# Performance work log

Hardware: AMD Instinct MI355X
Metric: run time of the kernel (lower is better)

The kernel has to match this reference:

```python
import jax, jax.numpy as jnp
import numpy as np

N, K, D = 16384, 2048, 512

def setup_inputs() -> dict:
    key = jax.random.key(0)
    kx, kmu, kstd = jax.random.split(key, 3)
    x = jax.random.normal(kx, (N, D), dtype=jnp.float32)
    mu = jax.random.normal(kmu, (K, D), dtype=jnp.float32)
    std = jax.random.uniform(kstd, (K, D), dtype=jnp.float32)  # positive so log(sum(std)) is defined
    return {"x": x, "mu": mu, "std": std}

def reference(x, mu, std):
    x_sq = jnp.sum(x * x, axis=1)                      # [N]
    mu_sq = jnp.sum(mu * mu, axis=1)                   # [K]
    sqdist = x_sq[:, None] - 2.0 * (x @ mu.T) + mu_sq[None, :]  # [N, K]
    denom = 2.0 * jnp.sum(std * std, axis=1) + 1e-8    # [K]
    log_std_sum = jnp.log(jnp.sum(std, axis=1))        # [K]
    half_log_2pi = 0.5 * jnp.log(jnp.asarray(2.0 * np.pi, dtype=x.dtype))
    return -sqdist / denom[None, :] - log_std_sum[None, :] - half_log_2pi
```

## Files before the change

kernel.cpp:

```cpp
#include <hip/hip_runtime.h>
#include <hip/hip_bf16.h>
#include <stdint.h>

#define NN 16384
#define KK 2048
#define DD 512

typedef __bf16 bf16x8 __attribute__((ext_vector_type(8)));
typedef float f32x4 __attribute__((ext_vector_type(4)));
typedef unsigned short ushort_t;
typedef ushort_t us8 __attribute__((ext_vector_type(8)));

#define AS1(p) ((const __attribute__((address_space(1))) void*)(p))
#define AS3(p) ((__attribute__((address_space(3))) void*)(p))

#define FENCE() asm volatile("" ::: "memory")
#define SBAR()  do { FENCE(); __builtin_amdgcn_s_barrier(); FENCE(); } while (0)
#define WAITVM0() asm volatile("s_waitcnt vmcnt(0)" ::: "memory")

__device__ inline ushort_t f2bf(float f) {
  uint32_t u = __float_as_uint(f);
  u += 0x7fffu + ((u >> 16) & 1u);
  return (ushort_t)(u >> 16);
}


__global__ __launch_bounds__(256) void prep_x(const float* __restrict__ x,
                                              ushort_t* __restrict__ xb,
                                              float* __restrict__ x_sq) {
  const int wave = threadIdx.x >> 6;
  const int lane = threadIdx.x & 63;
  const int row = blockIdx.x * 4 + wave;
  const float* xr = x + (size_t)row * DD + lane * 8;
  float4 v0 = *reinterpret_cast<const float4*>(xr);
  float4 v1 = *reinterpret_cast<const float4*>(xr + 4);
  float s = v0.x*v0.x + v0.y*v0.y + v0.z*v0.z + v0.w*v0.w
          + v1.x*v1.x + v1.y*v1.y + v1.z*v1.z + v1.w*v1.w;
  us8 o;
  o[0]=f2bf(v0.x); o[1]=f2bf(v0.y); o[2]=f2bf(v0.z); o[3]=f2bf(v0.w);
  o[4]=f2bf(v1.x); o[5]=f2bf(v1.y); o[6]=f2bf(v1.z); o[7]=f2bf(v1.w);

  const int br = row >> 8, m = (row >> 4) & 15, r = row & 15;
  const int kt = lane >> 3, cc2 = lane & 7, ks = cc2 >> 2, slot = cc2 & 3;
  size_t off = (size_t)(br * 8 + kt) * 16384 + (m * 2 + ks) * 512 + slot * 128 + r * 8;
  *reinterpret_cast<us8*>(xb + off) = o;

  #pragma unroll
  for (int offs = 32; offs; offs >>= 1) s += __shfl_xor(s, offs, 64);
  if (lane == 0) x_sq[row] = s;
}

__global__ __launch_bounds__(256) void prep_mu(const float* __restrict__ mu,
                                               const float* __restrict__ sd,
                                               ushort_t* __restrict__ mub,
                                               float* __restrict__ inv_denom,
                                               float* __restrict__ beta) {
  const int wave = threadIdx.x >> 6;
  const int lane = threadIdx.x & 63;
  const int row = blockIdx.x * 4 + wave;
  const float* mr = mu + (size_t)row * DD + lane * 8;
  float4 v0 = *reinterpret_cast<const float4*>(mr);
  float4 v1 = *reinterpret_cast<const float4*>(mr + 4);
  float musq = v0.x*v0.x + v0.y*v0.y + v0.z*v0.z + v0.w*v0.w
             + v1.x*v1.x + v1.y*v1.y + v1.z*v1.z + v1.w*v1.w;
  us8 o;
  o[0]=f2bf(v0.x); o[1]=f2bf(v0.y); o[2]=f2bf(v0.z); o[3]=f2bf(v0.w);
  o[4]=f2bf(v1.x); o[5]=f2bf(v1.y); o[6]=f2bf(v1.z); o[7]=f2bf(v1.w);

  const int bc = row >> 8, cB = (row >> 4) & 15, r = row & 15;
  const int kt = lane >> 3, cc2 = lane & 7, ks = cc2 >> 2, slot = cc2 & 3;
  size_t off = (size_t)(bc * 8 + kt) * 16384 + (cB * 2 + ks) * 512 + slot * 128 + r * 8;
  *reinterpret_cast<us8*>(mub + off) = o;

  const float* sr = sd + (size_t)row * DD + lane * 8;
  float4 s0 = *reinterpret_cast<const float4*>(sr);
  float4 s1 = *reinterpret_cast<const float4*>(sr + 4);
  float ssum = s0.x + s0.y + s0.z + s0.w + s1.x + s1.y + s1.z + s1.w;
  float ssq  = s0.x*s0.x + s0.y*s0.y + s0.z*s0.z + s0.w*s0.w
             + s1.x*s1.x + s1.y*s1.y + s1.z*s1.z + s1.w*s1.w;
  #pragma unroll
  for (int offs = 32; offs; offs >>= 1) {
    musq += __shfl_xor(musq, offs, 64);
    ssum += __shfl_xor(ssum, offs, 64);
    ssq  += __shfl_xor(ssq,  offs, 64);
  }
  if (lane == 0) {
    float idn = 1.0f / (2.0f * ssq + 1e-8f);
    inv_denom[row] = idn;
    beta[row] = musq * idn + logf(ssum) + 0.91893853320467274f;
  }
}

__global__ __launch_bounds__(512, 2) void gemm_eval(const ushort_t* __restrict__ xb,
                                                    const ushort_t* __restrict__ mub,
                                                    const float* __restrict__ x_sq,
                                                    const float* __restrict__ inv_denom,
                                                    const float* __restrict__ beta,
                                                    float* __restrict__ out) {
  __shared__ __align__(16) ushort_t As[2][16384];
  __shared__ __align__(16) ushort_t Bs[2][16384];

  const int t0 = threadIdx.x;
  const int lane = t0 & 63;
  const int w = t0 >> 6;
  const int wrow = w >> 2;
  const int wcol = w & 3;

  const int bid = blockIdx.x;
  const int swz = (bid & 7) * 64 + (bid >> 3);
  const int bm = swz >> 3, bn = swz & 7;

  const ushort_t* Ag = xb  + (size_t)bm * (8 * 16384);
  const ushort_t* Bg = mub + (size_t)bn * (8 * 16384);

  f32x4 acc[8][4];
  #pragma unroll
  for (int mmi = 0; mmi < 8; ++mmi)
    #pragma unroll
    for (int cc = 0; cc < 4; ++cc)
      acc[mmi][cc] = (f32x4){0.f, 0.f, 0.f, 0.f};

#define STAGE(kt, dbuf) do {                                                        \
    const ushort_t* as_ = Ag + (size_t)(kt) * 16384;                                \
    const ushort_t* bs_ = Bg + (size_t)(kt) * 16384;                                \
    ushort_t* ad_ = &As[dbuf][0];                                                   \
    ushort_t* bd_ = &Bs[dbuf][0];                                                   \
    __builtin_amdgcn_global_load_lds(AS1(as_ + t0*8),        AS3(ad_ + t0*8),        16, 0, 0); \
    __builtin_amdgcn_global_load_lds(AS1(as_ + (t0+512)*8),  AS3(ad_ + (t0+512)*8),  16, 0, 0); \
    __builtin_amdgcn_global_load_lds(AS1(as_ + (t0+1024)*8), AS3(ad_ + (t0+1024)*8), 16, 0, 0); \
    __builtin_amdgcn_global_load_lds(AS1(as_ + (t0+1536)*8), AS3(ad_ + (t0+1536)*8), 16, 0, 0); \
    __builtin_amdgcn_global_load_lds(AS1(bs_ + t0*8),        AS3(bd_ + t0*8),        16, 0, 0); \
    __builtin_amdgcn_global_load_lds(AS1(bs_ + (t0+512)*8),  AS3(bd_ + (t0+512)*8),  16, 0, 0); \
    __builtin_amdgcn_global_load_lds(AS1(bs_ + (t0+1024)*8), AS3(bd_ + (t0+1024)*8), 16, 0, 0); \
    __builtin_amdgcn_global_load_lds(AS1(bs_ + (t0+1536)*8), AS3(bd_ + (t0+1536)*8), 16, 0, 0); \
  } while (0)

  STAGE(0, 0);
  WAITVM0();
  SBAR();

  for (int t = 0; t < 8; ++t) {
    const ushort_t* Acur = &As[t & 1][0];
    const ushort_t* Bcur = &Bs[t & 1][0];
    bf16x8 bfrag[4][2];
    #pragma unroll
    for (int q = 0; q < 4; ++q) {
      bf16x8 af[2][2];
      #pragma unroll
      for (int i = 0; i < 2; ++i)
        #pragma unroll
        for (int ks = 0; ks < 2; ++ks)
          af[i][ks] = *reinterpret_cast<const bf16x8*>(
              Acur + ((wrow * 8 + q * 2 + i) * 2 + ks) * 512 + lane * 8);
      if (q == 0) {
        #pragma unroll
        for (int cc = 0; cc < 4; ++cc)
          #pragma unroll
          for (int ks = 0; ks < 2; ++ks)
            bfrag[cc][ks] = *reinterpret_cast<const bf16x8*>(
                Bcur + ((wcol * 4 + cc) * 2 + ks) * 512 + lane * 8);
        if (t < 7) STAGE(t + 1, (t + 1) & 1);
      }
      SBAR();
      __builtin_amdgcn_s_setprio(1);
      #pragma unroll
      for (int i = 0; i < 2; ++i)
        #pragma unroll
        for (int cc = 0; cc < 4; ++cc)
          #pragma unroll
          for (int ks = 0; ks < 2; ++ks)
            acc[q * 2 + i][cc] = __builtin_amdgcn_mfma_f32_16x16x32_bf16(
                af[i][ks], bfrag[cc][ks], acc[q * 2 + i][cc], 0, 0, 0);
      __builtin_amdgcn_s_setprio(0);
      if (q == 3) WAITVM0();
      SBAR();
    }
  }

  const int rl = lane & 15, rh = lane >> 4;
  const int colbase = bn * 256 + wcol * 64;
  float inv[4], bet[4];
  #pragma unroll
  for (int cc = 0; cc < 4; ++cc) {
    inv[cc] = inv_denom[colbase + cc * 16 + rl];
    bet[cc] = beta[colbase + cc * 16 + rl];
  }
  #pragma unroll
  for (int mmi = 0; mmi < 8; ++mmi) {
    const int nb = bm * 256 + wrow * 128 + mmi * 16 + rh * 4;
    #pragma unroll
    for (int reg = 0; reg < 4; ++reg) {
      const int n = nb + reg;
      const float xs = x_sq[n];
      float* op = out + (size_t)n * KK + colbase;
      #pragma unroll
      for (int cc = 0; cc < 4; ++cc)
        op[cc * 16 + rl] = (2.0f * acc[mmi][cc][reg] - xs) * inv[cc] - bet[cc];
    }
  }
#undef STAGE
}

extern "C" void kernel_launch(void* const* d_in, const int* in_sizes, int n_in,
                              void* d_out, int out_size, void* d_ws, size_t ws_size,
                              hipStream_t stream) {
  const float* x   = (const float*)d_in[0];
  const float* mu  = (const float*)d_in[1];
  const float* sd  = (const float*)d_in[2];
  float* out = (float*)d_out;

  char* ws = (char*)d_ws;
  ushort_t* xb        = (ushort_t*)(ws);
  ushort_t* mub       = (ushort_t*)(ws + 16777216);
  float*    x_sq      = (float*)(ws + 18874368);
  float*    inv_denom = (float*)(ws + 18939904);
  float*    beta      = (float*)(ws + 18948096);

  prep_x<<<NN / 4, 256, 0, stream>>>(x, xb, x_sq);
  prep_mu<<<KK / 4, 256, 0, stream>>>(mu, sd, mub, inv_denom, beta);
  gemm_eval<<<(NN / 256) * (KK / 256), 512, 0, stream>>>(xb, mub, x_sq, inv_denom, beta, out);
}
```

Measured before the change: 202.2 us.

## Switch GEMM to 4-stage K pipeline with smaller K tiles

Reorganizes the bf16 packed layout of x and mu into 32-wide K slices of 128-row images, and rewrites the GEMM main loop into a 4-buffer ring that keeps three K tiles in flight. A and B loads for the next-next tile are issued in separate halves of each step, with partial vmcnt waits instead of full drains. The aim is to hide global-to-LDS latency better than the old double buffer with its full wait each tile. In exchange it adds more barriers per unit of MFMA work (16 steps with 3 barriers each) and more complex vmcnt accounting.

```diff
diff --git a/kernel.cpp b/kernel.cpp
--- a/kernel.cpp
+++ b/kernel.cpp
@@ -13,10 +13,8 @@
 
 #define AS1(p) ((const __attribute__((address_space(1))) void*)(p))
 #define AS3(p) ((__attribute__((address_space(3))) void*)(p))
-
 #define FENCE() asm volatile("" ::: "memory")
 #define SBAR()  do { FENCE(); __builtin_amdgcn_s_barrier(); FENCE(); } while (0)
-#define WAITVM0() asm volatile("s_waitcnt vmcnt(0)" ::: "memory")
 
 __device__ inline ushort_t f2bf(float f) {
   uint32_t u = __float_as_uint(f);
@@ -40,9 +38,9 @@
   o[0]=f2bf(v0.x); o[1]=f2bf(v0.y); o[2]=f2bf(v0.z); o[3]=f2bf(v0.w);
   o[4]=f2bf(v1.x); o[5]=f2bf(v1.y); o[6]=f2bf(v1.z); o[7]=f2bf(v1.w);
 
-  const int br = row >> 8, m = (row >> 4) & 15, r = row & 15;
-  const int kt = lane >> 3, cc2 = lane & 7, ks = cc2 >> 2, slot = cc2 & 3;
-  size_t off = (size_t)(br * 8 + kt) * 16384 + (m * 2 + ks) * 512 + slot * 128 + r * 8;
+  const int br = row >> 7, m = (row >> 4) & 7, r = row & 15;
+  const int kt = lane >> 2, slot = lane & 3;
+  size_t off = ((size_t)(br * 16 + kt)) * 4096 + m * 512 + slot * 128 + r * 8;
   *reinterpret_cast<us8*>(xb + off) = o;
 
   #pragma unroll
@@ -67,9 +65,9 @@
   o[0]=f2bf(v0.x); o[1]=f2bf(v0.y); o[2]=f2bf(v0.z); o[3]=f2bf(v0.w);
   o[4]=f2bf(v1.x); o[5]=f2bf(v1.y); o[6]=f2bf(v1.z); o[7]=f2bf(v1.w);
 
-  const int bc = row >> 8, cB = (row >> 4) & 15, r = row & 15;
-  const int kt = lane >> 3, cc2 = lane & 7, ks = cc2 >> 2, slot = cc2 & 3;
-  size_t off = (size_t)(bc * 8 + kt) * 16384 + (cB * 2 + ks) * 512 + slot * 128 + r * 8;
+  const int bc = row >> 7, m = (row >> 4) & 7, r = row & 15;
+  const int kt = lane >> 2, slot = lane & 3;
+  size_t off = ((size_t)(bc * 16 + kt)) * 4096 + m * 512 + slot * 128 + r * 8;
   *reinterpret_cast<us8*>(mub + off) = o;
 
   const float* sr = sd + (size_t)row * DD + lane * 8;
@@ -97,8 +95,7 @@
                                                     const float* __restrict__ inv_denom,
                                                     const float* __restrict__ beta,
                                                     float* __restrict__ out) {
-  __shared__ __align__(16) ushort_t As[2][16384];
-  __shared__ __align__(16) ushort_t Bs[2][16384];
+  __shared__ __align__(16) ushort_t lds[4][16384];
 
   const int t0 = threadIdx.x;
   const int lane = t0 & 63;
@@ -110,72 +107,76 @@
   const int swz = (bid & 7) * 64 + (bid >> 3);
   const int bm = swz >> 3, bn = swz & 7;
 
-  const ushort_t* Ag = xb  + (size_t)bm * (8 * 16384);
-  const ushort_t* Bg = mub + (size_t)bn * (8 * 16384);
+  const ushort_t* Aimg0 = xb  + ((size_t)(bm * 2 + 0) * 16) * 4096;
+  const ushort_t* Aimg1 = xb  + ((size_t)(bm * 2 + 1) * 16) * 4096;
+  const ushort_t* Bimg0 = mub + ((size_t)(bn * 2 + 0) * 16) * 4096;
+  const ushort_t* Bimg1 = mub + ((size_t)(bn * 2 + 1) * 16) * 4096;
 
   f32x4 acc[8][4];
   #pragma unroll
-  for (int mmi = 0; mmi < 8; ++mmi)
+  for (int mm = 0; mm < 8; ++mm)
     #pragma unroll
     for (int cc = 0; cc < 4; ++cc)
-      acc[mmi][cc] = (f32x4){0.f, 0.f, 0.f, 0.f};
-
-#define STAGE(kt, dbuf) do {                                                        \
-    const ushort_t* as_ = Ag + (size_t)(kt) * 16384;                                \
-    const ushort_t* bs_ = Bg + (size_t)(kt) * 16384;                                \
-    ushort_t* ad_ = &As[dbuf][0];                                                   \
-    ushort_t* bd_ = &Bs[dbuf][0];                                                   \
-    __builtin_amdgcn_global_load_lds(AS1(as_ + t0*8),        AS3(ad_ + t0*8),        16, 0, 0); \
-    __builtin_amdgcn_global_load_lds(AS1(as_ + (t0+512)*8),  AS3(ad_ + (t0+512)*8),  16, 0, 0); \
-    __builtin_amdgcn_global_load_lds(AS1(as_ + (t0+1024)*8), AS3(ad_ + (t0+1024)*8), 16, 0, 0); \
-    __builtin_amdgcn_global_load_lds(AS1(as_ + (t0+1536)*8), AS3(ad_ + (t0+1536)*8), 16, 0, 0); \
-    __builtin_amdgcn_global_load_lds(AS1(bs_ + t0*8),        AS3(bd_ + t0*8),        16, 0, 0); \
-    __builtin_amdgcn_global_load_lds(AS1(bs_ + (t0+512)*8),  AS3(bd_ + (t0+512)*8),  16, 0, 0); \
-    __builtin_amdgcn_global_load_lds(AS1(bs_ + (t0+1024)*8), AS3(bd_ + (t0+1024)*8), 16, 0, 0); \
-    __builtin_amdgcn_global_load_lds(AS1(bs_ + (t0+1536)*8), AS3(bd_ + (t0+1536)*8), 16, 0, 0); \
+      acc[mm][cc] = (f32x4){0.f, 0.f, 0.f, 0.f};
+
+#define ISSUE_A(kt_, buf_) do {                                                                   \
+    __builtin_amdgcn_global_load_lds(AS1(Aimg0 + (size_t)(kt_) * 4096 + t0 * 8),                  \
+                                     AS3(&lds[buf_][0] + t0 * 8), 16, 0, 0);                      \
+    __builtin_amdgcn_global_load_lds(AS1(Aimg1 + (size_t)(kt_) * 4096 + t0 * 8),                  \
+                                     AS3(&lds[buf_][4096] + t0 * 8), 16, 0, 0);                   \
   } while (0)
-
-  STAGE(0, 0);
-  WAITVM0();
+#define ISSUE_B(kt_, buf_) do {                                                                   \
+    __builtin_amdgcn_global_load_lds(AS1(Bimg0 + (size_t)(kt_) * 4096 + t0 * 8),                  \
+                                     AS3(&lds[buf_][8192] + t0 * 8), 16, 0, 0);                   \
+    __builtin_amdgcn_global_load_lds(AS1(Bimg1 + (size_t)(kt_) * 4096 + t0 * 8),                  \
+                                     AS3(&lds[buf_][12288] + t0 * 8), 16, 0, 0);                  \
+  } while (0)
+
+#define TILE_BODY(t_, doIssue_, WAITASM) do {                                                     \
+    const int buf_ = (t_) & 3;                                                                    \
+    const ushort_t* Ab_ = &lds[buf_][wrow * 4096];                                                \
+    const ushort_t* Bb_ = &lds[buf_][8192 + (wcol >> 1) * 4096 + (wcol & 1) * 2048];              \
+    bf16x8 af_[4], bf_[4];                                                                        \
+    _Pragma("unroll") for (int i = 0; i < 4; ++i)                                                 \
+      af_[i] = *reinterpret_cast<const bf16x8*>(Ab_ + i * 512 + lane * 8);                        \
+    _Pragma("unroll") for (int c = 0; c < 4; ++c)                                                 \
+      bf_[c] = *reinterpret_cast<const bf16x8*>(Bb_ + c * 512 + lane * 8);                        \
+    if (doIssue_) ISSUE_A((t_) + 3, ((t_) + 3) & 3);                                              \
+    SBAR();                                                                                       \
+    __builtin_amdgcn_s_setprio(1);                                                                \
+    _Pragma("unroll") for (int i = 0; i < 4; ++i)                                                 \
+      _Pragma("unroll") for (int c = 0; c < 4; ++c)                                               \
+        acc[i][c] = __builtin_amdgcn_mfma_f32_16x16x32_bf16(af_[i], bf_[c], acc[i][c], 0, 0, 0);  \
+    __builtin_amdgcn_s_setprio(0);                                                                \
+    SBAR();                                                                                       \
+    _Pragma("unroll") for (int i = 0; i < 4; ++i)                                                 \
+      af_[i] = *reinterpret_cast<const bf16x8*>(Ab_ + (4 + i) * 512 + lane * 8);                  \
+    if (doIssue_) ISSUE_B((t_) + 3, ((t_) + 3) & 3);                                              \
+    SBAR();                                                                                       \
+    __builtin_amdgcn_s_setprio(1);                                                                \
+    _Pragma("unroll") for (int i = 0; i < 4; ++i)                                                 \
+      _Pragma("unroll") for (int c = 0; c < 4; ++c)                                               \
+        acc[4 + i][c] = __builtin_amdgcn_mfma_f32_16x16x32_bf16(af_[i], bf_[c], acc[4 + i][c], 0, 0, 0); \
+    __builtin_amdgcn_s_setprio(0);                                                                \
+    WAITASM;                                                                                      \
+    SBAR();                                                                                       \
+  } while (0)
+
+  ISSUE_A(0, 0); ISSUE_B(0, 0);
+  ISSUE_A(1, 1); ISSUE_B(1, 1);
+  ISSUE_A(2, 2); ISSUE_B(2, 2);
+  asm volatile("s_waitcnt vmcnt(8)" ::: "memory");
   SBAR();
 
-  for (int t = 0; t < 8; ++t) {
-    const ushort_t* Acur = &As[t & 1][0];
-    const ushort_t* Bcur = &Bs[t & 1][0];
-    bf16x8 bfrag[4][2];
-    #pragma unroll
-    for (int q = 0; q < 4; ++q) {
-      bf16x8 af[2][2];
-      #pragma unroll
-      for (int i = 0; i < 2; ++i)
-        #pragma unroll
-        for (int ks = 0; ks < 2; ++ks)
-          af[i][ks] = *reinterpret_cast<const bf16x8*>(
-              Acur + ((wrow * 8 + q * 2 + i) * 2 + ks) * 512 + lane * 8);
-      if (q == 0) {
-        #pragma unroll
-        for (int cc = 0; cc < 4; ++cc)
-          #pragma unroll
-          for (int ks = 0; ks < 2; ++ks)
-            bfrag[cc][ks] = *reinterpret_cast<const bf16x8*>(
-                Bcur + ((wcol * 4 + cc) * 2 + ks) * 512 + lane * 8);
-        if (t < 7) STAGE(t + 1, (t + 1) & 1);
-      }
-      SBAR();
-      __builtin_amdgcn_s_setprio(1);
-      #pragma unroll
-      for (int i = 0; i < 2; ++i)
-        #pragma unroll
-        for (int cc = 0; cc < 4; ++cc)
-          #pragma unroll
-          for (int ks = 0; ks < 2; ++ks)
-            acc[q * 2 + i][cc] = __builtin_amdgcn_mfma_f32_16x16x32_bf16(
-                af[i][ks], bfrag[cc][ks], acc[q * 2 + i][cc], 0, 0, 0);
-      __builtin_amdgcn_s_setprio(0);
-      if (q == 3) WAITVM0();
-      SBAR();
-    }
-  }
+  for (int t = 0; t < 13; ++t)
+    TILE_BODY(t, 1, asm volatile("s_waitcnt vmcnt(8)" ::: "memory"));
+  TILE_BODY(13, 0, asm volatile("s_waitcnt vmcnt(4)" ::: "memory"));
+  TILE_BODY(14, 0, asm volatile("s_waitcnt vmcnt(0)" ::: "memory"));
+  TILE_BODY(15, 0, (void)0);
+
+#undef TILE_BODY
+#undef ISSUE_A
+#undef ISSUE_B
 
   const int rl = lane & 15, rh = lane >> 4;
   const int colbase = bn * 256 + wcol * 64;
@@ -186,8 +187,8 @@
     bet[cc] = beta[colbase + cc * 16 + rl];
   }
   #pragma unroll
-  for (int mmi = 0; mmi < 8; ++mmi) {
-    const int nb = bm * 256 + wrow * 128 + mmi * 16 + rh * 4;
+  for (int mm = 0; mm < 8; ++mm) {
+    const int nb = bm * 256 + wrow * 128 + mm * 16 + rh * 4;
     #pragma unroll
     for (int reg = 0; reg < 4; ++reg) {
       const int n = nb + reg;
@@ -195,10 +196,9 @@
       float* op = out + (size_t)n * KK + colbase;
       #pragma unroll
       for (int cc = 0; cc < 4; ++cc)
-        op[cc * 16 + rl] = (2.0f * acc[mmi][cc][reg] - xs) * inv[cc] - bet[cc];
+        op[cc * 16 + rl] = (2.0f * acc[mm][cc][reg] - xs) * inv[cc] - bet[cc];
     }
   }
-#undef STAGE
 }
 
 extern "C" void kernel_launch(void* const* d_in, const int* in_sizes, int n_in,
```

New measurement: 199.3 us. No clear change (-1.5%).
